# Kernel tuning notes

Measured on AMD Instinct MI355X. Metric: run time of the kernel, lower is better.

Reference implementation:

```python
import jax, jax.numpy as jnp
import numpy as np

NUM_HEADS = 12
EPS = 1e-6

def setup_inputs() -> dict:
    key = jax.random.key(0)
    ks = jax.random.split(key, 7)
    B, N, C = 16, 4096, 384
    hd = C // NUM_HEADS
    s = 0.02
    return {
        "x": jax.random.normal(ks[0], (B, N, C), jnp.float32),
        "qkv_w": jax.random.normal(ks[1], (3 * C, C), jnp.float32) * s,
        "pos_enc": jax.random.normal(ks[2], (1, N, C), jnp.float32) * s,
        "dwc_w": jax.random.normal(ks[3], (hd, 1, 5, 5), jnp.float32) * s,
        "dwc_b": jnp.zeros((hd,), jnp.float32),
        "proj_w": jax.random.normal(ks[4], (C, C), jnp.float32) * s,
        "proj_b": jnp.zeros((C,), jnp.float32),
    }

def reference(x, qkv_w, pos_enc, dwc_w, dwc_b, proj_w, proj_b):
    B, N, C = x.shape
    H = NUM_HEADS
    hd = C // H
    qkv = x @ qkv_w.T  # (B, N, 3C)
    q, k, v = jnp.split(qkv, 3, axis=-1)
    k = k + pos_enc
    q = jax.nn.relu(q)
    k = jax.nn.relu(k)
    # b n (h c) -> (b h) n c
    def to_heads(t):
        return t.reshape(B, N, H, hd).transpose(0, 2, 1, 3).reshape(B * H, N, hd)
    q, k, v = to_heads(q), to_heads(k), to_heads(v)
    q = q.astype(jnp.float32); k = k.astype(jnp.float32); v = v.astype(jnp.float32)
    # normalizer z: (BH, N)
    z = 1.0 / (jnp.einsum('bic,bc->bi', q, k.sum(axis=1)) + EPS)
    # linear-attention branch (i*j*(c+d) > c*d*(i+j) here)
    kv = jnp.einsum('bjc,bjd->bcd', k, v)  # (BH, hd, hd)
    out = jnp.einsum('bic,bcd,bi->bid', q, kv, z)  # (BH, N, hd)
    # depthwise conv branch over v reshaped to spatial map
    w = int(np.sqrt(N))
    fm = v.reshape(B * H, w, w, hd).transpose(0, 3, 1, 2)  # b (w h) c -> b c w h
    fm = jax.lax.conv_general_dilated(
        fm, dwc_w, window_strides=(1, 1), padding=((2, 2), (2, 2)),
        feature_group_count=hd, dimension_numbers=('NCHW', 'OIHW', 'NCHW'))
    fm = fm + dwc_b[None, :, None, None]
    fm = fm.transpose(0, 2, 3, 1).reshape(B * H, N, hd)  # b c w h -> b (w h) c
    out = out + fm
    # (b h) n c -> b n (h c)
    out = out.reshape(B, H, N, hd).transpose(0, 2, 1, 3).reshape(B, N, C)
    return out @ proj_w.T + proj_b
```

## Files before the change

### kernel.cpp

```cpp
#include <hip/hip_runtime.h>
#include <hip/hip_bf16.h>
#include <cstdint>
#include <cstddef>


typedef __bf16 bf16;
typedef __attribute__((ext_vector_type(8))) __bf16 bf16x8;
typedef __attribute__((ext_vector_type(4))) __bf16 bf16x4;
typedef __attribute__((ext_vector_type(4))) float f32x4;
typedef __attribute__((ext_vector_type(16))) float f32x16;

#define NHEADS 12
#define HD 32
#define BATCH 16
#define SEQ 4096
#define CDIM 384
#define BHN (BATCH*NHEADS)
#define KVPARTS 2

__device__ __forceinline__ void gl_lds16(const bf16* g, bf16* l) {
    __builtin_amdgcn_global_load_lds(
        (const __attribute__((address_space(1))) unsigned int*)g,
        (__attribute__((address_space(3))) unsigned int*)l, 16, 0, 0);
}

__global__ void convert_in(const float* __restrict__ X, const float* __restrict__ qkvw,
                           const float* __restrict__ projw,
                           bf16* __restrict__ xb, bf16* __restrict__ qkvw_b,
                           bf16* __restrict__ projw_b) {
    int i = blockIdx.x * 256 + threadIdx.x;
    int stride = gridDim.x * 256;
    const int nx = (65536 * CDIM) / 8;
    for (int c = i; c < nx; c += stride) {
        const float* s = X + (size_t)c * 8;
        float4 f0 = *(const float4*)s;
        float4 f1 = *(const float4*)(s + 4);
        bf16x8 h;
        h[0]=(bf16)f0.x; h[1]=(bf16)f0.y; h[2]=(bf16)f0.z; h[3]=(bf16)f0.w;
        h[4]=(bf16)f1.x; h[5]=(bf16)f1.y; h[6]=(bf16)f1.z; h[7]=(bf16)f1.w;
        *(bf16x8*)&xb[(size_t)c * 8] = h;
    }
    const int nq = (3 * CDIM * CDIM) / 8;
    for (int c = i; c < nq; c += stride) {
        const float* s = qkvw + (size_t)c * 8;
        float4 f0 = *(const float4*)s;
        float4 f1 = *(const float4*)(s + 4);
        bf16x8 h;
        h[0]=(bf16)f0.x; h[1]=(bf16)f0.y; h[2]=(bf16)f0.z; h[3]=(bf16)f0.w;
        h[4]=(bf16)f1.x; h[5]=(bf16)f1.y; h[6]=(bf16)f1.z; h[7]=(bf16)f1.w;
        *(bf16x8*)&qkvw_b[(size_t)c * 8] = h;
    }
    const int np = (CDIM * CDIM) / 8;
    for (int c = i; c < np; c += stride) {
        const float* s = projw + (size_t)c * 8;
        float4 f0 = *(const float4*)s;
        float4 f1 = *(const float4*)(s + 4);
        bf16x8 h;
        h[0]=(bf16)f0.x; h[1]=(bf16)f0.y; h[2]=(bf16)f0.z; h[3]=(bf16)f0.w;
        h[4]=(bf16)f1.x; h[5]=(bf16)f1.y; h[6]=(bf16)f1.z; h[7]=(bf16)f1.w;
        *(bf16x8*)&projw_b[(size_t)c * 8] = h;
    }
}

__global__ __launch_bounds__(256, 2)
void gemm_qkv(const bf16* __restrict__ X, const bf16* __restrict__ Wb,
              const float* __restrict__ pos,
              bf16* __restrict__ qh, bf16* __restrict__ kh, bf16* __restrict__ vh) {
    __shared__ bf16 As[128 * 64];
    __shared__ bf16 Bs[128 * 64];
    const int tid  = threadIdx.x;
    const int lane = tid & 63;
    const int wid  = tid >> 6;
    const int blk  = blockIdx.x;
    const int work = (blk & 7) * (4608 / 8) + (blk >> 3);
    const int mt   = work / 9;
    const int nt   = work - mt * 9;
    const int m0   = mt * 128;
    const int n0   = nt * 128;
    const int wm   = (wid & 1) * 64;
    const int wn   = (wid >> 1) * 64;
    const int lr   = lane & 15;
    const int lq   = lane >> 4;

    const int srow = (lane >> 3);
    const int sc   = lane & 7;

    f32x4 acc[4][4] = {};

    for (int k0 = 0; k0 < CDIM; k0 += 64) {
        #pragma unroll
        for (int it = 0; it < 4; ++it) {
            int rbase = wid * 32 + it * 8;
            int r = rbase + srow;
            int gc = sc ^ (r & 7);
            gl_lds16(&X [(size_t)(m0 + r) * CDIM + k0 + gc * 8], &As[rbase * 64]);
            gl_lds16(&Wb[(size_t)(n0 + r) * CDIM + k0 + gc * 8], &Bs[rbase * 64]);
        }
        __syncthreads();
        #pragma unroll
        for (int ks = 0; ks < 2; ++ks) {
            bf16x8 af[4], bfr[4];
            #pragma unroll
            for (int mi = 0; mi < 4; ++mi) {
                int r = wm + mi * 16 + lr;
                af[mi] = *(const bf16x8*)&As[r * 64 + ((ks * 4 + lq) ^ (r & 7)) * 8];
            }
            #pragma unroll
            for (int ni = 0; ni < 4; ++ni) {
                int r = wn + ni * 16 + lr;
                bfr[ni] = *(const bf16x8*)&Bs[r * 64 + ((ks * 4 + lq) ^ (r & 7)) * 8];
            }
            #pragma unroll
            for (int mi = 0; mi < 4; ++mi)
                #pragma unroll
                for (int ni = 0; ni < 4; ++ni)
                    acc[mi][ni] = __builtin_amdgcn_mfma_f32_16x16x32_bf16(
                        af[mi], bfr[ni], acc[mi][ni], 0, 0, 0);
        }
        __syncthreads();
    }

    const int sec = n0 / CDIM;
    #pragma unroll
    for (int mi = 0; mi < 4; ++mi) {
        #pragma unroll
        for (int ni = 0; ni < 4; ++ni) {
            int n = n0 + wn + ni * 16 + lr;
            int c = n - sec * CDIM;
            int hh = c >> 5, d = c & 31;
            #pragma unroll
            for (int r = 0; r < 4; ++r) {
                int m = m0 + wm + mi * 16 + lq * 4 + r;
                int b = m >> 12, i = m & 4095;
                float v = acc[mi][ni][r];
                size_t dst = ((size_t)(b * NHEADS + hh) * SEQ + i) * HD + d;
                if (sec == 0) {
                    qh[dst] = (bf16)fmaxf(v, 0.f);
                } else if (sec == 1) {
                    v += pos[(size_t)i * CDIM + c];
                    kh[dst] = (bf16)fmaxf(v, 0.f);
                } else {
                    vh[dst] = (bf16)v;
                }
            }
        }
    }
}

__global__ __launch_bounds__(256, 2)
void kv_mfma(const bf16* __restrict__ kh, const bf16* __restrict__ vh,
             float* __restrict__ kv_part, float* __restrict__ ksum_part) {
    __shared__ float red[4 * 1024];
    __shared__ float ksred[4 * 32];
    const int tid  = threadIdx.x;
    const int lane = tid & 63;
    const int w    = tid >> 6;
    const int bh   = blockIdx.y;
    const int part = blockIdx.x;
    const int col  = lane & 31;
    const int half = lane >> 5;
    const bf16* kb = kh + (size_t)bh * SEQ * HD;
    const bf16* vb = vh + (size_t)bh * SEQ * HD;
    const int j0 = part * 2048 + w * 512;

    f32x16 acc = {};
    f32x16 aks = {};
    bf16x8 ones;
    #pragma unroll
    for (int j = 0; j < 8; ++j) ones[j] = (bf16)1.0f;

    for (int s = 0; s < 32; ++s) {
        int jb = j0 + s * 16 + half * 8;
        bf16x8 afr, bfr;
        #pragma unroll
        for (int j = 0; j < 8; ++j) {
            afr[j] = kb[(size_t)(jb + j) * HD + col];
            bfr[j] = vb[(size_t)(jb + j) * HD + col];
        }
        acc = __builtin_amdgcn_mfma_f32_32x32x16_bf16(afr, bfr, acc, 0, 0, 0);
        aks = __builtin_amdgcn_mfma_f32_32x32x16_bf16(afr, ones, aks, 0, 0, 0);
    }

    #pragma unroll
    for (int r = 0; r < 16; ++r) {
        int row = (r & 3) + 8 * (r >> 2) + 4 * half;
        red[w * 1024 + row * 32 + col] = acc[r];
        ksred[w * 32 + row] = aks[r];
    }
    __syncthreads();
    {
        int e = tid * 4;
        f32x4 s4 = *(f32x4*)&red[e];
        s4 += *(f32x4*)&red[1024 + e];
        s4 += *(f32x4*)&red[2048 + e];
        s4 += *(f32x4*)&red[3072 + e];
        *(f32x4*)&kv_part[((size_t)bh * KVPARTS + part) * 1024 + e] = s4;
    }
    if (tid < 32) {
        ksum_part[((size_t)bh * KVPARTS + part) * 32 + tid] =
            ksred[tid] + ksred[32 + tid] + ksred[64 + tid] + ksred[96 + tid];
    }
}

__global__ __launch_bounds__(256, 2)
void attn_out(const bf16* __restrict__ qh, const bf16* __restrict__ vh,
              const float* __restrict__ kv_part, const float* __restrict__ ksum_part,
              const float* __restrict__ dwcw, const float* __restrict__ dwcb,
              bf16* __restrict__ outp) {
    __shared__ bf16 vt[12 * 64 * 32];
    __shared__ float kvl[1024];
    __shared__ float ksl[32];
    __shared__ float wl[25 * 32];
    __shared__ float bl[32];
    const int tid = threadIdx.x;
    const int bh  = blockIdx.y;
    const int ys  = blockIdx.x * 8;
    const bf16* vbase = vh + (size_t)bh * SEQ * HD;

    #pragma unroll
    for (int it = 0; it < 12; ++it) {
        int cid = tid + it * 256;
        int vy = cid >> 8;
        int xx = (cid >> 2) & 63;
        int q  = cid & 3;
        int gy = ys + vy - 2;
        bf16x8 val = {};
        if (gy >= 0 && gy < 64)
            val = *(const bf16x8*)&vbase[((size_t)gy * 64 + xx) * HD + q * 8];
        *(bf16x8*)&vt[(vy * 64 + xx) * HD + q * 8] = val;
    }
    {
        const float* kp = kv_part + (size_t)bh * KVPARTS * 1024;
        f32x4 t = *(const f32x4*)&kp[tid * 4];
        t += *(const f32x4*)&kp[1024 + tid * 4];
        *(f32x4*)&kvl[tid * 4] = t;
    }
    if (tid < 32) {
        const float* sp = ksum_part + (size_t)bh * KVPARTS * 32;
        ksl[tid] = sp[tid] + sp[32 + tid];
        #pragma unroll
        for (int tap = 0; tap < 25; ++tap) wl[tap * 32 + tid] = dwcw[tid * 25 + tap];
        bl[tid] = dwcb[tid];
    }
    __syncthreads();

    const int dq = tid & 7, d0 = dq * 4;
    const int ri = tid >> 3;
    const int b = bh / NHEADS, hh = bh % NHEADS;
    const bf16* qbase = qh + (size_t)bh * SEQ * HD;

    for (int it = 0; it < 16; ++it) {
        int pix = ri + it * 32;
        int yy = pix >> 6;
        int x  = pix & 63;
        int tok = (ys + yy) * 64 + x;
        float zden = 1e-6f;
        float dot0 = 0, dot1 = 0, dot2 = 0, dot3 = 0;
        #pragma unroll
        for (int c4 = 0; c4 < 32; c4 += 4) {
            bf16x4 qv = *(const bf16x4*)&qbase[(size_t)tok * HD + c4];
            #pragma unroll
            for (int u = 0; u < 4; ++u) {
                float qf = (float)qv[u];
                int c = c4 + u;
                zden += qf * ksl[c];
                dot0 += qf * kvl[c * 32 + d0];
                dot1 += qf * kvl[c * 32 + d0 + 1];
                dot2 += qf * kvl[c * 32 + d0 + 2];
                dot3 += qf * kvl[c * 32 + d0 + 3];
            }
        }
        float z = 1.f / zden;
        float f0 = bl[d0], f1 = bl[d0 + 1], f2 = bl[d0 + 2], f3 = bl[d0 + 3];
        int vyc = yy + 2;
        #pragma unroll
        for (int dy = -2; dy <= 2; ++dy) {
            #pragma unroll
            for (int dx = -2; dx <= 2; ++dx) {
                int xx = x + dx;
                if (xx < 0 || xx >= 64) continue;
                int tap = (dy + 2) * 5 + (dx + 2);
                bf16x4 vv = *(const bf16x4*)&vt[((vyc + dy) * 64 + xx) * HD + d0];
                const float* wp = &wl[tap * 32 + d0];
                f0 += (float)vv[0] * wp[0];
                f1 += (float)vv[1] * wp[1];
                f2 += (float)vv[2] * wp[2];
                f3 += (float)vv[3] * wp[3];
            }
        }
        bf16x4 ov;
        ov[0] = (bf16)(dot0 * z + f0);
        ov[1] = (bf16)(dot1 * z + f1);
        ov[2] = (bf16)(dot2 * z + f2);
        ov[3] = (bf16)(dot3 * z + f3);
        *(bf16x4*)&outp[((size_t)b * SEQ + tok) * CDIM + hh * HD + d0] = ov;
    }
}

__global__ __launch_bounds__(256, 2)
void gemm_proj(const bf16* __restrict__ A, const bf16* __restrict__ Wb,
               const float* __restrict__ bias, float* __restrict__ out) {
    __shared__ bf16 As[128 * 64];
    __shared__ bf16 Bs[128 * 64];
    const int tid  = threadIdx.x;
    const int lane = tid & 63;
    const int wid  = tid >> 6;
    const int blk  = blockIdx.x;
    const int work = (blk & 7) * (1536 / 8) + (blk >> 3);
    const int mt   = work / 3;
    const int nt   = work - mt * 3;
    const int m0   = mt * 128;
    const int n0   = nt * 128;
    const int wm   = (wid & 1) * 64;
    const int wn   = (wid >> 1) * 64;
    const int lr   = lane & 15;
    const int lq   = lane >> 4;
    const int srow = (lane >> 3);
    const int sc   = lane & 7;

    f32x4 acc[4][4] = {};

    for (int k0 = 0; k0 < CDIM; k0 += 64) {
        #pragma unroll
        for (int it = 0; it < 4; ++it) {
            int rbase = wid * 32 + it * 8;
            int r = rbase + srow;
            int gc = sc ^ (r & 7);
            gl_lds16(&A [(size_t)(m0 + r) * CDIM + k0 + gc * 8], &As[rbase * 64]);
            gl_lds16(&Wb[(size_t)(n0 + r) * CDIM + k0 + gc * 8], &Bs[rbase * 64]);
        }
        __syncthreads();
        #pragma unroll
        for (int ks = 0; ks < 2; ++ks) {
            bf16x8 af[4], bfr[4];
            #pragma unroll
            for (int mi = 0; mi < 4; ++mi) {
                int r = wm + mi * 16 + lr;
                af[mi] = *(const bf16x8*)&As[r * 64 + ((ks * 4 + lq) ^ (r & 7)) * 8];
            }
            #pragma unroll
            for (int ni = 0; ni < 4; ++ni) {
                int r = wn + ni * 16 + lr;
                bfr[ni] = *(const bf16x8*)&Bs[r * 64 + ((ks * 4 + lq) ^ (r & 7)) * 8];
            }
            #pragma unroll
            for (int mi = 0; mi < 4; ++mi)
                #pragma unroll
                for (int ni = 0; ni < 4; ++ni)
                    acc[mi][ni] = __builtin_amdgcn_mfma_f32_16x16x32_bf16(
                        af[mi], bfr[ni], acc[mi][ni], 0, 0, 0);
        }
        __syncthreads();
    }

    #pragma unroll
    for (int mi = 0; mi < 4; ++mi) {
        #pragma unroll
        for (int ni = 0; ni < 4; ++ni) {
            int n = n0 + wn + ni * 16 + lr;
            float bv = bias[n];
            #pragma unroll
            for (int r = 0; r < 4; ++r) {
                int m = m0 + wm + mi * 16 + lq * 4 + r;
                out[(size_t)m * CDIM + n] = acc[mi][ni][r] + bv;
            }
        }
    }
}

extern "C" void kernel_launch(void* const* d_in, const int* in_sizes, int n_in,
                              void* d_out, int out_size, void* d_ws, size_t ws_size,
                              hipStream_t stream) {
    const float* x     = (const float*)d_in[0];
    const float* qkvw  = (const float*)d_in[1];
    const float* pos   = (const float*)d_in[2];
    const float* dwcw  = (const float*)d_in[3];
    const float* dwcb  = (const float*)d_in[4];
    const float* projw = (const float*)d_in[5];
    const float* projb = (const float*)d_in[6];
    float* out = (float*)d_out;

    char* ws = (char*)d_ws;
    size_t off = 0;
    auto alloc = [&](size_t bytes) -> void* {
        void* p = ws + off;
        off += (bytes + 255) & ~(size_t)255;
        return p;
    };
    bf16* xb      = (bf16*)alloc((size_t)65536 * CDIM * 2);
    bf16* qkvw_b  = (bf16*)alloc((size_t)3 * CDIM * CDIM * 2);
    bf16* projw_b = (bf16*)alloc((size_t)CDIM * CDIM * 2);
    bf16* qh  = (bf16*)alloc((size_t)BHN * SEQ * HD * 2);
    bf16* khb = (bf16*)alloc((size_t)BHN * SEQ * HD * 2);
    bf16* vh  = (bf16*)alloc((size_t)BHN * SEQ * HD * 2);
    float* kvb   = (float*)alloc((size_t)BHN * KVPARTS * HD * HD * 4);
    float* ksumb = (float*)alloc((size_t)BHN * KVPARTS * HD * 4);

    hipLaunchKernelGGL(convert_in, dim3(2048), dim3(256), 0, stream,
                       x, qkvw, projw, xb, qkvw_b, projw_b);
    hipLaunchKernelGGL(gemm_qkv, dim3(4608), dim3(256), 0, stream,
                       xb, qkvw_b, pos, qh, khb, vh);
    hipLaunchKernelGGL(kv_mfma, dim3(KVPARTS, BHN), dim3(256), 0, stream,
                       khb, vh, kvb, ksumb);
    bf16* outp = khb;
    hipLaunchKernelGGL(attn_out, dim3(8, BHN), dim3(256), 0, stream,
                       qh, vh, kvb, ksumb, dwcw, dwcb, outp);
    hipLaunchKernelGGL(gemm_proj, dim3(1536), dim3(256), 0, stream,
                       outp, projw_b, projb, out);
}
```

Baseline: 475.6 us.

## Enlarge GEMM tiles, split KV reduction further, and move attention output to MFMA

Both GEMMs move from 128x128 to 256x128 tiles held in one shared buffer, with each wave owning 64 rows across all 128 columns. This raises operand reuse per LDS load and halves the grid. The KV reduction is split into 4 parts for more parallelism, and attn_out now computes q·kv and the normalizer with MFMA instructions instead of scalar FMAs. In attn_out the depthwise convolution is computed first into a shared buffer with 8-wide vectors, using smaller row tiles. The cost is more registers per thread (a 4x8 accumulator array), bf16 rounding of kv/ksum and the conv result, and an extra pass through LDS.

```diff
diff --git a/kernel.cpp b/kernel.cpp
--- a/kernel.cpp
+++ b/kernel.cpp
@@ -16,7 +16,7 @@
 #define SEQ 4096
 #define CDIM 384
 #define BHN (BATCH*NHEADS)
-#define KVPARTS 2
+#define KVPARTS 4
 
 __device__ __forceinline__ void gl_lds16(const bf16* g, bf16* l) {
     __builtin_amdgcn_global_load_lds(
@@ -66,54 +66,52 @@
 void gemm_qkv(const bf16* __restrict__ X, const bf16* __restrict__ Wb,
               const float* __restrict__ pos,
               bf16* __restrict__ qh, bf16* __restrict__ kh, bf16* __restrict__ vh) {
-    __shared__ bf16 As[128 * 64];
-    __shared__ bf16 Bs[128 * 64];
+    __shared__ bf16 sh[384 * 64];
     const int tid  = threadIdx.x;
     const int lane = tid & 63;
     const int wid  = tid >> 6;
     const int blk  = blockIdx.x;
-    const int work = (blk & 7) * (4608 / 8) + (blk >> 3);
+    const int work = (blk & 7) * (2304 / 8) + (blk >> 3);
     const int mt   = work / 9;
     const int nt   = work - mt * 9;
-    const int m0   = mt * 128;
+    const int m0   = mt * 256;
     const int n0   = nt * 128;
-    const int wm   = (wid & 1) * 64;
-    const int wn   = (wid >> 1) * 64;
     const int lr   = lane & 15;
     const int lq   = lane >> 4;
-
-    const int srow = (lane >> 3);
+    const int srow = lane >> 3;
     const int sc   = lane & 7;
 
-    f32x4 acc[4][4] = {};
+    f32x4 acc[4][8] = {};
 
     for (int k0 = 0; k0 < CDIM; k0 += 64) {
         #pragma unroll
-        for (int it = 0; it < 4; ++it) {
-            int rbase = wid * 32 + it * 8;
-            int r = rbase + srow;
-            int gc = sc ^ (r & 7);
-            gl_lds16(&X [(size_t)(m0 + r) * CDIM + k0 + gc * 8], &As[rbase * 64]);
-            gl_lds16(&Wb[(size_t)(n0 + r) * CDIM + k0 + gc * 8], &Bs[rbase * 64]);
+        for (int it = 0; it < 12; ++it) {
+            int rbase = wid * 96 + it * 8;
+            int g = rbase + srow;
+            int gc = sc ^ (g & 7);
+            const bf16* src = (g < 256)
+                ? &X [(size_t)(m0 + g) * CDIM + k0 + gc * 8]
+                : &Wb[(size_t)(n0 + g - 256) * CDIM + k0 + gc * 8];
+            gl_lds16(src, &sh[rbase * 64]);
         }
         __syncthreads();
         #pragma unroll
         for (int ks = 0; ks < 2; ++ks) {
-            bf16x8 af[4], bfr[4];
+            bf16x8 af[4], bfr[8];
             #pragma unroll
             for (int mi = 0; mi < 4; ++mi) {
-                int r = wm + mi * 16 + lr;
-                af[mi] = *(const bf16x8*)&As[r * 64 + ((ks * 4 + lq) ^ (r & 7)) * 8];
-            }
-            #pragma unroll
-            for (int ni = 0; ni < 4; ++ni) {
-                int r = wn + ni * 16 + lr;
-                bfr[ni] = *(const bf16x8*)&Bs[r * 64 + ((ks * 4 + lq) ^ (r & 7)) * 8];
+                int r = wid * 64 + mi * 16 + lr;
+                af[mi] = *(const bf16x8*)&sh[r * 64 + ((ks * 4 + lq) ^ (r & 7)) * 8];
+            }
+            #pragma unroll
+            for (int ni = 0; ni < 8; ++ni) {
+                int r = 256 + ni * 16 + lr;
+                bfr[ni] = *(const bf16x8*)&sh[r * 64 + ((ks * 4 + lq) ^ (r & 7)) * 8];
             }
             #pragma unroll
             for (int mi = 0; mi < 4; ++mi)
                 #pragma unroll
-                for (int ni = 0; ni < 4; ++ni)
+                for (int ni = 0; ni < 8; ++ni)
                     acc[mi][ni] = __builtin_amdgcn_mfma_f32_16x16x32_bf16(
                         af[mi], bfr[ni], acc[mi][ni], 0, 0, 0);
         }
@@ -124,13 +122,13 @@
     #pragma unroll
     for (int mi = 0; mi < 4; ++mi) {
         #pragma unroll
-        for (int ni = 0; ni < 4; ++ni) {
-            int n = n0 + wn + ni * 16 + lr;
+        for (int ni = 0; ni < 8; ++ni) {
+            int n = n0 + ni * 16 + lr;
             int c = n - sec * CDIM;
             int hh = c >> 5, d = c & 31;
             #pragma unroll
             for (int r = 0; r < 4; ++r) {
-                int m = m0 + wm + mi * 16 + lq * 4 + r;
+                int m = m0 + wid * 64 + mi * 16 + lq * 4 + r;
                 int b = m >> 12, i = m & 4095;
                 float v = acc[mi][ni][r];
                 size_t dst = ((size_t)(b * NHEADS + hh) * SEQ + i) * HD + d;
@@ -161,7 +159,7 @@
     const int half = lane >> 5;
     const bf16* kb = kh + (size_t)bh * SEQ * HD;
     const bf16* vb = vh + (size_t)bh * SEQ * HD;
-    const int j0 = part * 2048 + w * 512;
+    const int j0 = part * 1024 + w * 256;
 
     f32x16 acc = {};
     f32x16 aks = {};
@@ -169,7 +167,8 @@
     #pragma unroll
     for (int j = 0; j < 8; ++j) ones[j] = (bf16)1.0f;
 
-    for (int s = 0; s < 32; ++s) {
+    #pragma unroll 2
+    for (int s = 0; s < 16; ++s) {
         int jb = j0 + s * 16 + half * 8;
         bf16x8 afr, bfr;
         #pragma unroll
@@ -207,18 +206,22 @@
               const float* __restrict__ kv_part, const float* __restrict__ ksum_part,
               const float* __restrict__ dwcw, const float* __restrict__ dwcb,
               bf16* __restrict__ outp) {
-    __shared__ bf16 vt[12 * 64 * 32];
+    __shared__ bf16 vt[8 * 64 * 32];
+    __shared__ bf16 convres[256 * 32];
     __shared__ float kvl[1024];
     __shared__ float ksl[32];
     __shared__ float wl[25 * 32];
     __shared__ float bl[32];
-    const int tid = threadIdx.x;
-    const int bh  = blockIdx.y;
-    const int ys  = blockIdx.x * 8;
+    const int tid  = threadIdx.x;
+    const int lane = tid & 63;
+    const int wid  = tid >> 6;
+    const int bh   = blockIdx.y;
+    const int ys   = blockIdx.x * 4;
     const bf16* vbase = vh + (size_t)bh * SEQ * HD;
-
-    #pragma unroll
-    for (int it = 0; it < 12; ++it) {
+    const bf16* qbase = qh + (size_t)bh * SEQ * HD;
+
+    #pragma unroll
+    for (int it = 0; it < 8; ++it) {
         int cid = tid + it * 256;
         int vy = cid >> 8;
         int xx = (cid >> 2) & 63;
@@ -233,120 +236,140 @@
         const float* kp = kv_part + (size_t)bh * KVPARTS * 1024;
         f32x4 t = *(const f32x4*)&kp[tid * 4];
         t += *(const f32x4*)&kp[1024 + tid * 4];
+        t += *(const f32x4*)&kp[2048 + tid * 4];
+        t += *(const f32x4*)&kp[3072 + tid * 4];
         *(f32x4*)&kvl[tid * 4] = t;
     }
     if (tid < 32) {
         const float* sp = ksum_part + (size_t)bh * KVPARTS * 32;
-        ksl[tid] = sp[tid] + sp[32 + tid];
+        ksl[tid] = sp[tid] + sp[32 + tid] + sp[64 + tid] + sp[96 + tid];
         #pragma unroll
         for (int tap = 0; tap < 25; ++tap) wl[tap * 32 + tid] = dwcw[tid * 25 + tap];
         bl[tid] = dwcb[tid];
     }
     __syncthreads();
 
-    const int dq = tid & 7, d0 = dq * 4;
-    const int ri = tid >> 3;
+    {
+        const int d0 = (tid & 3) * 8;
+        const int ri = tid >> 2;
+        #pragma unroll
+        for (int it = 0; it < 4; ++it) {
+            int pix = ri + it * 64;
+            int yy = pix >> 6;
+            int x  = pix & 63;
+            float f[8];
+            #pragma unroll
+            for (int dd = 0; dd < 8; ++dd) f[dd] = bl[d0 + dd];
+            int vyc = yy + 2;
+            #pragma unroll
+            for (int dy = -2; dy <= 2; ++dy) {
+                #pragma unroll
+                for (int dx = -2; dx <= 2; ++dx) {
+                    int xx = x + dx;
+                    if (xx < 0 || xx >= 64) continue;
+                    int tap = (dy + 2) * 5 + (dx + 2);
+                    bf16x8 vv = *(const bf16x8*)&vt[((vyc + dy) * 64 + xx) * HD + d0];
+                    const float* wp = &wl[tap * 32 + d0];
+                    #pragma unroll
+                    for (int dd = 0; dd < 8; ++dd) f[dd] += (float)vv[dd] * wp[dd];
+                }
+            }
+            bf16x8 cv;
+            #pragma unroll
+            for (int dd = 0; dd < 8; ++dd) cv[dd] = (bf16)f[dd];
+            *(bf16x8*)&convres[pix * HD + d0] = cv;
+        }
+    }
+    __syncthreads();
+
+    const int col  = lane & 31;
+    const int half = lane >> 5;
     const int b = bh / NHEADS, hh = bh % NHEADS;
-    const bf16* qbase = qh + (size_t)bh * SEQ * HD;
-
-    for (int it = 0; it < 16; ++it) {
-        int pix = ri + it * 32;
-        int yy = pix >> 6;
-        int x  = pix & 63;
-        int tok = (ys + yy) * 64 + x;
-        float zden = 1e-6f;
-        float dot0 = 0, dot1 = 0, dot2 = 0, dot3 = 0;
-        #pragma unroll
-        for (int c4 = 0; c4 < 32; c4 += 4) {
-            bf16x4 qv = *(const bf16x4*)&qbase[(size_t)tok * HD + c4];
-            #pragma unroll
-            for (int u = 0; u < 4; ++u) {
-                float qf = (float)qv[u];
-                int c = c4 + u;
-                zden += qf * ksl[c];
-                dot0 += qf * kvl[c * 32 + d0];
-                dot1 += qf * kvl[c * 32 + d0 + 1];
-                dot2 += qf * kvl[c * 32 + d0 + 2];
-                dot3 += qf * kvl[c * 32 + d0 + 3];
-            }
-        }
-        float z = 1.f / zden;
-        float f0 = bl[d0], f1 = bl[d0 + 1], f2 = bl[d0 + 2], f3 = bl[d0 + 3];
-        int vyc = yy + 2;
-        #pragma unroll
-        for (int dy = -2; dy <= 2; ++dy) {
-            #pragma unroll
-            for (int dx = -2; dx <= 2; ++dx) {
-                int xx = x + dx;
-                if (xx < 0 || xx >= 64) continue;
-                int tap = (dy + 2) * 5 + (dx + 2);
-                bf16x4 vv = *(const bf16x4*)&vt[((vyc + dy) * 64 + xx) * HD + d0];
-                const float* wp = &wl[tap * 32 + d0];
-                f0 += (float)vv[0] * wp[0];
-                f1 += (float)vv[1] * wp[1];
-                f2 += (float)vv[2] * wp[2];
-                f3 += (float)vv[3] * wp[3];
-            }
-        }
-        bf16x4 ov;
-        ov[0] = (bf16)(dot0 * z + f0);
-        ov[1] = (bf16)(dot1 * z + f1);
-        ov[2] = (bf16)(dot2 * z + f2);
-        ov[3] = (bf16)(dot3 * z + f3);
-        *(bf16x4*)&outp[((size_t)b * SEQ + tok) * CDIM + hh * HD + d0] = ov;
+
+    bf16x8 bkv0, bkv1, bks0, bks1;
+    #pragma unroll
+    for (int j = 0; j < 8; ++j) {
+        int k = half * 8 + j;
+        bkv0[j] = (bf16)kvl[k * 32 + col];
+        bkv1[j] = (bf16)kvl[(16 + k) * 32 + col];
+        bks0[j] = (bf16)ksl[k];
+        bks1[j] = (bf16)ksl[16 + k];
+    }
+
+    #pragma unroll
+    for (int t = 0; t < 2; ++t) {
+        int mt = wid * 2 + t;
+        int tok0 = ys * 64 + mt * 32;
+        int tokL = tok0 + col;
+        bf16x8 a0 = *(const bf16x8*)&qbase[(size_t)tokL * HD + half * 8];
+        bf16x8 a1 = *(const bf16x8*)&qbase[(size_t)tokL * HD + 16 + half * 8];
+        f32x16 acc = {};
+        f32x16 den = {};
+        acc = __builtin_amdgcn_mfma_f32_32x32x16_bf16(a0, bkv0, acc, 0, 0, 0);
+        acc = __builtin_amdgcn_mfma_f32_32x32x16_bf16(a1, bkv1, acc, 0, 0, 0);
+        den = __builtin_amdgcn_mfma_f32_32x32x16_bf16(a0, bks0, den, 0, 0, 0);
+        den = __builtin_amdgcn_mfma_f32_32x32x16_bf16(a1, bks1, den, 0, 0, 0);
+        #pragma unroll
+        for (int r = 0; r < 16; ++r) {
+            int row = (r & 3) + 8 * (r >> 2) + 4 * half;
+            int pix = mt * 32 + row;
+            int tok = ys * 64 + pix;
+            float z = 1.f / (den[r] + 1e-6f);
+            float val = acc[r] * z + (float)convres[pix * HD + col];
+            outp[((size_t)b * SEQ + tok) * CDIM + hh * HD + col] = (bf16)val;
+        }
     }
 }
 
 __global__ __launch_bounds__(256, 2)
 void gemm_proj(const bf16* __restrict__ A, const bf16* __restrict__ Wb,
                const float* __restrict__ bias, float* __restrict__ out) {
-    __shared__ bf16 As[128 * 64];
-    __shared__ bf16 Bs[128 * 64];
+    __shared__ bf16 sh[384 * 64];
     const int tid  = threadIdx.x;
     const int lane = tid & 63;
     const int wid  = tid >> 6;
     const int blk  = blockIdx.x;
-    const int work = (blk & 7) * (1536 / 8) + (blk >> 3);
+    const int work = (blk & 7) * (768 / 8) + (blk >> 3);
     const int mt   = work / 3;
     const int nt   = work - mt * 3;
-    const int m0   = mt * 128;
+    const int m0   = mt * 256;
     const int n0   = nt * 128;
-    const int wm   = (wid & 1) * 64;
-    const int wn   = (wid >> 1) * 64;
     const int lr   = lane & 15;
     const int lq   = lane >> 4;
-    const int srow = (lane >> 3);
+    const int srow = lane >> 3;
     const int sc   = lane & 7;
 
-    f32x4 acc[4][4] = {};
+    f32x4 acc[4][8] = {};
 
     for (int k0 = 0; k0 < CDIM; k0 += 64) {
         #pragma unroll
-        for (int it = 0; it < 4; ++it) {
-            int rbase = wid * 32 + it * 8;
-            int r = rbase + srow;
-            int gc = sc ^ (r & 7);
-            gl_lds16(&A [(size_t)(m0 + r) * CDIM + k0 + gc * 8], &As[rbase * 64]);
-            gl_lds16(&Wb[(size_t)(n0 + r) * CDIM + k0 + gc * 8], &Bs[rbase * 64]);
+        for (int it = 0; it < 12; ++it) {
+            int rbase = wid * 96 + it * 8;
+            int g = rbase + srow;
+            int gc = sc ^ (g & 7);
+            const bf16* src = (g < 256)
+                ? &A [(size_t)(m0 + g) * CDIM + k0 + gc * 8]
+                : &Wb[(size_t)(n0 + g - 256) * CDIM + k0 + gc * 8];
+            gl_lds16(src, &sh[rbase * 64]);
         }
         __syncthreads();
         #pragma unroll
         for (int ks = 0; ks < 2; ++ks) {
-            bf16x8 af[4], bfr[4];
+            bf16x8 af[4], bfr[8];
             #pragma unroll
             for (int mi = 0; mi < 4; ++mi) {
-                int r = wm + mi * 16 + lr;
-                af[mi] = *(const bf16x8*)&As[r * 64 + ((ks * 4 + lq) ^ (r & 7)) * 8];
-            }
-            #pragma unroll
-            for (int ni = 0; ni < 4; ++ni) {
-                int r = wn + ni * 16 + lr;
-                bfr[ni] = *(const bf16x8*)&Bs[r * 64 + ((ks * 4 + lq) ^ (r & 7)) * 8];
+                int r = wid * 64 + mi * 16 + lr;
+                af[mi] = *(const bf16x8*)&sh[r * 64 + ((ks * 4 + lq) ^ (r & 7)) * 8];
+            }
+            #pragma unroll
+            for (int ni = 0; ni < 8; ++ni) {
+                int r = 256 + ni * 16 + lr;
+                bfr[ni] = *(const bf16x8*)&sh[r * 64 + ((ks * 4 + lq) ^ (r & 7)) * 8];
             }
             #pragma unroll
             for (int mi = 0; mi < 4; ++mi)
                 #pragma unroll
-                for (int ni = 0; ni < 4; ++ni)
+                for (int ni = 0; ni < 8; ++ni)
                     acc[mi][ni] = __builtin_amdgcn_mfma_f32_16x16x32_bf16(
                         af[mi], bfr[ni], acc[mi][ni], 0, 0, 0);
         }
@@ -356,12 +379,12 @@
     #pragma unroll
     for (int mi = 0; mi < 4; ++mi) {
         #pragma unroll
-        for (int ni = 0; ni < 4; ++ni) {
-            int n = n0 + wn + ni * 16 + lr;
+        for (int ni = 0; ni < 8; ++ni) {
+            int n = n0 + ni * 16 + lr;
             float bv = bias[n];
             #pragma unroll
             for (int r = 0; r < 4; ++r) {
-                int m = m0 + wm + mi * 16 + lq * 4 + r;
+                int m = m0 + wid * 64 + mi * 16 + lq * 4 + r;
                 out[(size_t)m * CDIM + n] = acc[mi][ni][r] + bv;
             }
         }
@@ -398,13 +421,13 @@
 
     hipLaunchKernelGGL(convert_in, dim3(2048), dim3(256), 0, stream,
                        x, qkvw, projw, xb, qkvw_b, projw_b);
-    hipLaunchKernelGGL(gemm_qkv, dim3(4608), dim3(256), 0, stream,
+    hipLaunchKernelGGL(gemm_qkv, dim3(2304), dim3(256), 0, stream,
                        xb, qkvw_b, pos, qh, khb, vh);
     hipLaunchKernelGGL(kv_mfma, dim3(KVPARTS, BHN), dim3(256), 0, stream,
                        khb, vh, kvb, ksumb);
     bf16* outp = khb;
-    hipLaunchKernelGGL(attn_out, dim3(8, BHN), dim3(256), 0, stream,
+    hipLaunchKernelGGL(attn_out, dim3(16, BHN), dim3(256), 0, stream,
                        qh, vh, kvb, ksumb, dwcw, dwcb, outp);
-    hipLaunchKernelGGL(gemm_proj, dim3(1536), dim3(256), 0, stream,
+    hipLaunchKernelGGL(gemm_proj, dim3(768), dim3(256), 0, stream,
                        outp, projw_b, projb, out);
 }
```

After: 478.6 us. About the same (+0.6%).
